# Kernel tuning notes

Hardware: AMD Instinct MI355X
Metric: run time of the kernel (lower is better)

The kernel has to match this reference:

```python
import jax, jax.numpy as jnp
import numpy as np

NUM_HEADS = 16


def setup_inputs() -> dict:
    B, S, A, H = 2, 2048, 16, 1024
    key = jax.random.key(0)
    k1, k2, k3, k4, k5, k6 = jax.random.split(key, 6)
    h1 = jax.random.normal(k1, (B, S, H), dtype=jnp.float32)
    h2 = jax.random.normal(k2, (B, A, H), dtype=jnp.float32)
    # variable-length boolean masks (at least one valid position per row)
    sent_len = jax.random.randint(k3, (B,), S // 2, S + 1)
    sentence_mask = jnp.arange(S)[None, :] < sent_len[:, None]
    asp_len = jax.random.randint(k4, (B,), 1, A + 1)
    aspect_mask = jnp.arange(A)[None, :] < asp_len[:, None]
    # xavier-uniform-ish init for Linear weights stored torch-style [out, in]
    bound = float(np.sqrt(6.0 / (H + H)))
    Wq = jax.random.uniform(k5, (H, H), jnp.float32, -bound, bound)
    Wk = jax.random.uniform(k6, (H, H), jnp.float32, -bound, bound)
    return {"h1": h1, "h2": h2, "sentence_mask": sentence_mask,
            "aspect_mask": aspect_mask, "Wq": Wq, "Wk": Wk}


def reference(h1, h2, sentence_mask, aspect_mask, Wq, Wk):
    B, S, H = h1.shape
    hd = H // NUM_HEADS
    scale = hd ** -0.5

    # --- masked mean aggregation of aspect features: [B, A, H] -> [B, H] ---
    m = aspect_mask.astype(h2.dtype)                      # [B, A]
    lengths = jnp.clip(m.sum(axis=1, keepdims=True), 1.0)  # [B, 1]
    h2_agg = (h2 * m[..., None]).sum(axis=1) / lengths     # [B, H]

    # query = aggregated aspect broadcast over seq positions: [B, S, H]
    h3 = jnp.broadcast_to(h2_agg[:, None, :], (B, S, H))

    # Linear (no bias), torch convention y = x @ W^T
    Q = jnp.einsum('bsh,oh->bso', h3, Wq)                  # [B, S, H]
    K = jnp.einsum('bsh,oh->bso', h1, Wk)                  # [B, S, H]

    Qh = Q.reshape(B, S, NUM_HEADS, hd)                    # [B, S, nh, hd]
    Kh = K.reshape(B, S, NUM_HEADS, hd)

    # scaled dot-product scores: [B, nh, S, S]
    scores = jnp.einsum('bqhd,bkhd->bhqk', Qh, Kh) * scale

    # key-side mask: broadcast [B, S] over (heads, query) dims
    scores = jnp.where(sentence_mask[:, None, None, :], scores, -jnp.inf)

    weights = jax.nn.softmax(scores, axis=-1)              # [B, nh, S, S]
    attention_matrix = weights.mean(axis=1)                # [B, S, S]
    return attention_matrix
```

## Files before the change

### kernel.cpp

```cpp
#include <hip/hip_runtime.h>

#define B 2
#define S 2048
#define A 16
#define H 1024
#define NH 16
#define HD 64
#define KT 16
#define HG 8
#define CH 4
#define QC 16
#define KC 1024

__global__ __launch_bounds__(256) void kQW(const float* __restrict__ h2,
                                           const int* __restrict__ amask,
                                           const float* __restrict__ Wq,
                                           const float* __restrict__ Wk,
                                           float* __restrict__ weff) {
    __shared__ float agg[H];
    __shared__ float qs[HD];
    int blk = blockIdx.x;
    int c = blk & (CH - 1);
    int bh = blk / CH;
    int b = bh >> 4, h = bh & 15;
    int tid = threadIdx.x;

    {
        const float4* h2b = (const float4*)(h2 + (size_t)b * A * H);
        float4 sum = make_float4(0.f, 0.f, 0.f, 0.f);
        int cnt = 0;
#pragma unroll
        for (int a = 0; a < A; a++) {
            if (amask[b * A + a]) {
                float4 v = h2b[a * (H / 4) + tid];
                sum.x += v.x; sum.y += v.y; sum.z += v.z; sum.w += v.w; cnt++;
            }
        }
        float inv = 1.0f / (float)(cnt > 0 ? cnt : 1);
        ((float4*)agg)[tid] = make_float4(sum.x * inv, sum.y * inv, sum.z * inv, sum.w * inv);
    }
    __syncthreads();

    int wave = tid >> 6, lane = tid & 63;
    const float4* ag = (const float4*)agg;
    for (int d = wave * 16; d < wave * 16 + 16; d++) {
        const float4* wr = (const float4*)(Wq + (size_t)(h * HD + d) * H);
        float acc = 0.f;
#pragma unroll
        for (int t = 0; t < 4; t++) {
            int j4 = lane + 64 * t;
            float4 a4 = ag[j4], w4 = wr[j4];
            acc += a4.x * w4.x + a4.y * w4.y + a4.z * w4.z + a4.w * w4.w;
        }
        for (int off = 32; off > 0; off >>= 1) acc += __shfl_down(acc, off);
        if (lane == 0) qs[d] = acc;
    }
    __syncthreads();

    int j = c * 256 + tid;
    float acc = 0.f;
#pragma unroll 8
    for (int d = 0; d < HD; d++) acc += qs[d] * Wk[(size_t)(h * HD + d) * H + j];
    weff[((size_t)b * NH + h) * H + j] = acc * 0.125f;
}

__global__ __launch_bounds__(256) void kB(const float* __restrict__ h1,
                                          const float* __restrict__ weff,
                                          float* __restrict__ s) {
    __shared__ float4 lw[HG * H / 4];
    int blk = blockIdx.x;
    int hg = blk & 1;
    int rest = blk >> 1;
    int kt = rest % (S / KT);
    int b  = rest / (S / KT);
    const float4* wsrc = (const float4*)(weff + ((size_t)b * NH + hg * HG) * H);
    for (int i = threadIdx.x; i < HG * H / 4; i += 256) lw[i] = wsrc[i];
    __syncthreads();

    int wave = threadIdx.x >> 6, lane = threadIdx.x & 63;
    for (int kl = wave; kl < KT; kl += 4) {
        int k = kt * KT + kl;
        const float4* row = (const float4*)(h1 + ((size_t)b * S + k) * H);
        float4 x[4];
#pragma unroll
        for (int t = 0; t < 4; t++) x[t] = row[lane + 64 * t];
#pragma unroll
        for (int hh = 0; hh < HG; hh++) {
            float acc = 0.f;
#pragma unroll
            for (int t = 0; t < 4; t++) {
                float4 wv = lw[hh * (H / 4) + lane + 64 * t];
                acc += wv.x * x[t].x + wv.y * x[t].y + wv.z * x[t].z + wv.w * x[t].w;
            }
            for (int off = 32; off > 0; off >>= 1) acc += __shfl_down(acc, off);
            if (lane == 0) s[((size_t)b * NH + hg * HG + hh) * S + k] = acc;
        }
    }
}

__global__ __launch_bounds__(256) void kS(const float* __restrict__ s,
                                          const int* __restrict__ smask,
                                          float* __restrict__ m,
                                          float* __restrict__ dsum) {
    __shared__ float red[4];
    int bh = blockIdx.x, b = bh >> 4;
    int tid = threadIdx.x, wave = tid >> 6, lane = tid & 63;
    const float4* srow = (const float4*)(s + (size_t)bh * S);
    const int4* mrow = (const int4*)(smask + b * S);

    float mx = -3.4e38f;
#pragma unroll
    for (int t = 0; t < 2; t++) {
        int i = tid + 256 * t;
        float4 v = srow[i]; int4 mk = mrow[i];
        if (mk.x) mx = fmaxf(mx, v.x);
        if (mk.y) mx = fmaxf(mx, v.y);
        if (mk.z) mx = fmaxf(mx, v.z);
        if (mk.w) mx = fmaxf(mx, v.w);
    }
    for (int off = 32; off > 0; off >>= 1) mx = fmaxf(mx, __shfl_down(mx, off));
    if (lane == 0) red[wave] = mx;
    __syncthreads();
    float gmax = fmaxf(fmaxf(red[0], red[1]), fmaxf(red[2], red[3]));
    __syncthreads();

    float sum = 0.f;
#pragma unroll
    for (int t = 0; t < 2; t++) {
        int i = tid + 256 * t;
        float4 v = srow[i]; int4 mk = mrow[i];
        if (mk.x) sum += expf(v.x - gmax);
        if (mk.y) sum += expf(v.y - gmax);
        if (mk.z) sum += expf(v.z - gmax);
        if (mk.w) sum += expf(v.w - gmax);
    }
    for (int off = 32; off > 0; off >>= 1) sum += __shfl_down(sum, off);
    if (lane == 0) red[wave] = sum;
    __syncthreads();
    if (tid == 0) { m[bh] = gmax; dsum[bh] = red[0] + red[1] + red[2] + red[3]; }
}

__global__ __launch_bounds__(256) void kD(const float* __restrict__ s,
                                          const int* __restrict__ smask,
                                          const float* __restrict__ m,
                                          const float* __restrict__ dsum,
                                          float* __restrict__ out) {
    __shared__ float wch[KC];
    int blk = blockIdx.x;
    int b  = blk >> 8;
    int r  = blk & 255;
    int kc = r >> 7;
    int q0 = (r & 127) * QC;
    int tid = threadIdx.x;

    float mh[NH], ih[NH];
#pragma unroll
    for (int h = 0; h < NH; h++) {
        mh[h] = m[b * NH + h];
        ih[h] = 1.0f / dsum[b * NH + h];
    }

    {
        int k = kc * KC + tid * 4;
        int4 mk = *(const int4*)(smask + b * S + k);
        float4 val = make_float4(0.f, 0.f, 0.f, 0.f);
#pragma unroll
        for (int h = 0; h < NH; h++) {
            float4 sv = *(const float4*)(s + ((size_t)b * NH + h) * S + k);
            val.x += expf(sv.x - mh[h]) * ih[h];
            val.y += expf(sv.y - mh[h]) * ih[h];
            val.z += expf(sv.z - mh[h]) * ih[h];
            val.w += expf(sv.w - mh[h]) * ih[h];
        }
        const float inh = 1.0f / NH;
        val.x = mk.x ? val.x * inh : 0.f;
        val.y = mk.y ? val.y * inh : 0.f;
        val.z = mk.z ? val.z * inh : 0.f;
        val.w = mk.w ? val.w * inh : 0.f;
        ((float4*)wch)[tid] = val;
    }
    __syncthreads();

    float4 v = ((float4*)wch)[tid];
#pragma unroll
    for (int qi = 0; qi < QC; qi++) {
        float4* dst = (float4*)(out + ((size_t)(b * S + q0 + qi)) * S + kc * KC);
        dst[tid] = v;
    }
}

extern "C" void kernel_launch(void* const* d_in, const int* in_sizes, int n_in,
                              void* d_out, int out_size, void* d_ws, size_t ws_size,
                              hipStream_t stream) {
    const float* h1    = (const float*)d_in[0];
    const float* h2    = (const float*)d_in[1];
    const int*   smask = (const int*)d_in[2];
    const int*   amask = (const int*)d_in[3];
    const float* Wq    = (const float*)d_in[4];
    const float* Wk    = (const float*)d_in[5];
    float* out = (float*)d_out;
    float* ws  = (float*)d_ws;

    float* weff = ws;
    float* s    = ws + 32768;
    float* m    = ws + 98304;
    float* dsum = ws + 98336;

    kQW<<<B * NH * CH, 256, 0, stream>>>(h2, amask, Wq, Wk, weff);
    kB <<<B * (S / KT) * 2, 256, 0, stream>>>(h1, weff, s);
    kS <<<B * NH, 256, 0, stream>>>(s, smask, m, dsum);
    kD <<<B * (S / KC) * (S / QC), 256, 0, stream>>>(s, smask, m, dsum, out);
}
```

Measured before the change: 118.7 us.

## Fuse softmax statistics into score kernel via per-tile partial max/sum

Drops the separate softmax-statistics kernel. The score kernel now computes a masked partial max and exp-sum for each 16-key tile and head. The final kernel merges these partials with an online-softmax rescale before writing the averaged weights. This removes one launch and a serial low-parallelism pass, but every output block now redundantly reads and reduces 128 partials per head.

```diff
diff --git a/kernel.cpp b/kernel.cpp
--- a/kernel.cpp
+++ b/kernel.cpp
@@ -11,6 +11,7 @@
 #define CH 4
 #define QC 16
 #define KC 1024
+#define NKT (S / KT)
 
 __global__ __launch_bounds__(256) void kQW(const float* __restrict__ h2,
                                            const int* __restrict__ amask,
@@ -66,15 +67,21 @@
 
 __global__ __launch_bounds__(256) void kB(const float* __restrict__ h1,
                                           const float* __restrict__ weff,
-                                          float* __restrict__ s) {
+                                          const int* __restrict__ smask,
+                                          float* __restrict__ s,
+                                          float* __restrict__ pmax,
+                                          float* __restrict__ psum) {
     __shared__ float4 lw[HG * H / 4];
+    __shared__ float s_tile[HG][KT];
+    __shared__ int mk_tile[KT];
     int blk = blockIdx.x;
     int hg = blk & 1;
     int rest = blk >> 1;
-    int kt = rest % (S / KT);
-    int b  = rest / (S / KT);
+    int kt = rest % NKT;
+    int b  = rest / NKT;
     const float4* wsrc = (const float4*)(weff + ((size_t)b * NH + hg * HG) * H);
     for (int i = threadIdx.x; i < HG * H / 4; i += 256) lw[i] = wsrc[i];
+    if (threadIdx.x < KT) mk_tile[threadIdx.x] = smask[b * S + kt * KT + threadIdx.x];
     __syncthreads();
 
     int wave = threadIdx.x >> 6, lane = threadIdx.x & 63;
@@ -93,72 +100,60 @@
                 acc += wv.x * x[t].x + wv.y * x[t].y + wv.z * x[t].z + wv.w * x[t].w;
             }
             for (int off = 32; off > 0; off >>= 1) acc += __shfl_down(acc, off);
-            if (lane == 0) s[((size_t)b * NH + hg * HG + hh) * S + k] = acc;
-        }
-    }
-}
-
-__global__ __launch_bounds__(256) void kS(const float* __restrict__ s,
-                                          const int* __restrict__ smask,
-                                          float* __restrict__ m,
-                                          float* __restrict__ dsum) {
-    __shared__ float red[4];
-    int bh = blockIdx.x, b = bh >> 4;
-    int tid = threadIdx.x, wave = tid >> 6, lane = tid & 63;
-    const float4* srow = (const float4*)(s + (size_t)bh * S);
-    const int4* mrow = (const int4*)(smask + b * S);
-
-    float mx = -3.4e38f;
-#pragma unroll
-    for (int t = 0; t < 2; t++) {
-        int i = tid + 256 * t;
-        float4 v = srow[i]; int4 mk = mrow[i];
-        if (mk.x) mx = fmaxf(mx, v.x);
-        if (mk.y) mx = fmaxf(mx, v.y);
-        if (mk.z) mx = fmaxf(mx, v.z);
-        if (mk.w) mx = fmaxf(mx, v.w);
-    }
-    for (int off = 32; off > 0; off >>= 1) mx = fmaxf(mx, __shfl_down(mx, off));
-    if (lane == 0) red[wave] = mx;
-    __syncthreads();
-    float gmax = fmaxf(fmaxf(red[0], red[1]), fmaxf(red[2], red[3]));
-    __syncthreads();
-
-    float sum = 0.f;
-#pragma unroll
-    for (int t = 0; t < 2; t++) {
-        int i = tid + 256 * t;
-        float4 v = srow[i]; int4 mk = mrow[i];
-        if (mk.x) sum += expf(v.x - gmax);
-        if (mk.y) sum += expf(v.y - gmax);
-        if (mk.z) sum += expf(v.z - gmax);
-        if (mk.w) sum += expf(v.w - gmax);
-    }
-    for (int off = 32; off > 0; off >>= 1) sum += __shfl_down(sum, off);
-    if (lane == 0) red[wave] = sum;
-    __syncthreads();
-    if (tid == 0) { m[bh] = gmax; dsum[bh] = red[0] + red[1] + red[2] + red[3]; }
+            if (lane == 0) {
+                s[((size_t)b * NH + hg * HG + hh) * S + k] = acc;
+                s_tile[hh][kl] = acc;
+            }
+        }
+    }
+    __syncthreads();
+
+    if (threadIdx.x < HG) {
+        int hh = threadIdx.x;
+        float mx = -3.4e38f;
+#pragma unroll
+        for (int i = 0; i < KT; i++) if (mk_tile[i]) mx = fmaxf(mx, s_tile[hh][i]);
+        float sum = 0.f;
+#pragma unroll
+        for (int i = 0; i < KT; i++) if (mk_tile[i]) sum += expf(s_tile[hh][i] - mx);
+        int idx = ((b * NH + hg * HG + hh) * NKT) + kt;
+        pmax[idx] = mx;
+        psum[idx] = sum;
+    }
 }
 
 __global__ __launch_bounds__(256) void kD(const float* __restrict__ s,
                                           const int* __restrict__ smask,
-                                          const float* __restrict__ m,
-                                          const float* __restrict__ dsum,
+                                          const float* __restrict__ pmax,
+                                          const float* __restrict__ psum,
                                           float* __restrict__ out) {
     __shared__ float wch[KC];
+    __shared__ float mh_s[NH], ih_s[NH];
     int blk = blockIdx.x;
     int b  = blk >> 8;
     int r  = blk & 255;
     int kc = r >> 7;
     int q0 = (r & 127) * QC;
-    int tid = threadIdx.x;
+    int tid = threadIdx.x, wave = tid >> 6, lane = tid & 63;
+
+#pragma unroll
+    for (int hh = 0; hh < 4; hh++) {
+        int h = wave * 4 + hh;
+        int base = (b * NH + h) * NKT;
+        float m1 = pmax[base + lane], m2 = pmax[base + 64 + lane];
+        float mx = fmaxf(m1, m2);
+        for (int off = 32; off > 0; off >>= 1) mx = fmaxf(mx, __shfl_down(mx, off));
+        mx = __shfl(mx, 0);
+        float sum = psum[base + lane] * expf(m1 - mx)
+                  + psum[base + 64 + lane] * expf(m2 - mx);
+        for (int off = 32; off > 0; off >>= 1) sum += __shfl_down(sum, off);
+        if (lane == 0) { mh_s[h] = mx; ih_s[h] = 1.0f / sum; }
+    }
+    __syncthreads();
 
     float mh[NH], ih[NH];
 #pragma unroll
-    for (int h = 0; h < NH; h++) {
-        mh[h] = m[b * NH + h];
-        ih[h] = 1.0f / dsum[b * NH + h];
-    }
+    for (int h = 0; h < NH; h++) { mh[h] = mh_s[h]; ih[h] = ih_s[h]; }
 
     {
         int k = kc * KC + tid * 4;
@@ -203,11 +198,10 @@
 
     float* weff = ws;
     float* s    = ws + 32768;
-    float* m    = ws + 98304;
-    float* dsum = ws + 98336;
+    float* pmax = ws + 98304;
+    float* psum = ws + 102400;
 
     kQW<<<B * NH * CH, 256, 0, stream>>>(h2, amask, Wq, Wk, weff);
-    kB <<<B * (S / KT) * 2, 256, 0, stream>>>(h1, weff, s);
-    kS <<<B * NH, 256, 0, stream>>>(s, smask, m, dsum);
-    kD <<<B * (S / KC) * (S / QC), 256, 0, stream>>>(s, smask, m, dsum, out);
-}
+    kB <<<B * NKT * 2, 256, 0, stream>>>(h1, weff, smask, s, pmax, psum);
+    kD <<<B * (S / KC) * (S / QC), 256, 0, stream>>>(s, smask, pmax, psum, out);
+}
```

Result: slower. 123.3 us (+3.9%).
